# Optimization experiments

Hardware: AMD Instinct MI355X
Metric: run time of the kernel (lower is better)

Reference implementation:

```python
import jax, jax.numpy as jnp
import numpy as np

N_NODES = 50000
NUM_LAYERS = 3
D = 128
NUM_LABELS = 16
NUM_EDGES = 1600000


def setup_inputs() -> dict:
    key = jax.random.key(0)
    ks = jax.random.split(key, 6)
    s = 1.0 / np.sqrt(D)
    x = jax.random.normal(ks[0], (N_NODES, D), dtype=jnp.float32)
    edge_index = jax.random.randint(ks[1], (2, NUM_EDGES), 0, N_NODES, dtype=jnp.int64)
    W1 = jax.random.normal(ks[2], (NUM_LAYERS, D, D), dtype=jnp.float32) * s
    b1 = jnp.zeros((NUM_LAYERS, D), dtype=jnp.float32)
    W2 = jax.random.normal(ks[3], (NUM_LAYERS, D, D), dtype=jnp.float32) * s
    b2 = jnp.zeros((NUM_LAYERS, D), dtype=jnp.float32)
    Wc = jax.random.normal(ks[4], (D, NUM_LABELS), dtype=jnp.float32) * s
    bc = jnp.zeros((NUM_LABELS,), dtype=jnp.float32)
    return {"x": x, "edge_index": edge_index, "W1": W1, "b1": b1,
            "W2": W2, "b2": b2, "Wc": Wc, "bc": bc}


def reference(x, edge_index, W1, b1, W2, b2, Wc, bc):
    # PyG GINConv (default eps=0): h_i = MLP((1+eps)*x_i + sum_{j->i} x_j)
    src, dst = edge_index[0], edge_index[1]
    h = x
    for l in range(NUM_LAYERS):
        agg = jax.ops.segment_sum(h[src], dst, num_segments=N_NODES)  # [N, D]
        z = h + agg
        h = jax.nn.relu(z @ W1[l] + b1[l]) @ W2[l] + b2[l]
    logits = h @ Wc + bc
    return (h, logits)
```

## Files before the change

### kernel.cpp

```cpp
#include <hip/hip_runtime.h>

#define DD 128
#define CHUNK 6144
#define NBMAX 512
#define SCAP 8192

typedef __attribute__((ext_vector_type(8))) short bf16x8;
typedef __attribute__((ext_vector_type(4))) float f32x4;

__device__ __forceinline__ unsigned bf16rne(float f) {
  unsigned u = __float_as_uint(f);
  return (u + 0x7FFFu + ((u >> 16) & 1u)) >> 16;
}
__device__ __forceinline__ unsigned packbf(float lo, float hi) {
  return bf16rne(lo) | (bf16rne(hi) << 16);
}
__device__ __forceinline__ float bflo(unsigned v) { return __uint_as_float(v << 16); }
__device__ __forceinline__ float bfhi(unsigned v) { return __uint_as_float(v & 0xFFFF0000u); }

__device__ void block_scan_incl(int* cnt, int* inc, int nb, int tid) {
  for (int i = tid; i < nb; i += 256) inc[i] = cnt[i];
  __syncthreads();
  for (int d = 1; d < nb; d <<= 1) {
    int i0 = tid, i1 = tid + 256;
    int v0 = 0, v1 = 0;
    if (i0 < nb && i0 >= d) v0 = inc[i0 - d];
    if (i1 < nb && i1 >= d) v1 = inc[i1 - d];
    __syncthreads();
    if (i0 < nb) inc[i0] += v0;
    if (i1 < nb) inc[i1] += v1;
    __syncthreads();
  }
}

__global__ __launch_bounds__(256) void s1_hist(const int* __restrict__ dst,
                                               int* __restrict__ bucketCount, int e) {
  __shared__ int h[NBMAX];
  int tid = threadIdx.x;
  for (int i = tid; i < NBMAX; i += 256) h[i] = 0;
  __syncthreads();
  int i0 = blockIdx.x * CHUNK;
  int i1 = min(i0 + CHUNK, e);
  for (int i = i0 + tid; i < i1; i += 256) atomicAdd(&h[dst[i] >> 7], 1);
  __syncthreads();
  for (int i = tid; i < NBMAX; i += 256)
    if (h[i]) atomicAdd(&bucketCount[i], h[i]);
}

__global__ __launch_bounds__(256) void s2_scan(const int* __restrict__ bucketCount,
                                               int* __restrict__ bucketOff,
                                               int* __restrict__ gCursor,
                                               int* __restrict__ rs, int nb, int n, int e) {
  __shared__ int cnt[NBMAX], inc[NBMAX];
  int tid = threadIdx.x;
  for (int i = tid; i < nb; i += 256) cnt[i] = bucketCount[i];
  __syncthreads();
  block_scan_incl(cnt, inc, nb, tid);
  for (int i = tid; i < nb; i += 256) {
    int off = inc[i] - cnt[i];
    bucketOff[i] = off;
    gCursor[i] = off;
  }
  if (tid == 0) { bucketOff[nb] = e; rs[n] = e; }
}

__global__ __launch_bounds__(256) void s3_scatter(const int* __restrict__ src,
                                                  const int* __restrict__ dst,
                                                  int* __restrict__ gCursor,
                                                  unsigned int* __restrict__ bucketed,
                                                  int e, int nb) {
  __shared__ int cnt[NBMAX], inc[NBMAX], base[NBMAX], cur[NBMAX];
  __shared__ unsigned int pairs[CHUNK];
  int tid = threadIdx.x;
  for (int i = tid; i < nb; i += 256) cnt[i] = 0;
  __syncthreads();
  int i0 = blockIdx.x * CHUNK;
  int i1 = min(i0 + CHUNK, e);
  for (int i = i0 + tid; i < i1; i += 256) atomicAdd(&cnt[dst[i] >> 7], 1);
  __syncthreads();
  block_scan_incl(cnt, inc, nb, tid);
  for (int b = tid; b < nb; b += 256) {
    int c = cnt[b];
    base[b] = c ? atomicAdd(&gCursor[b], c) : 0;
    cur[b] = inc[b] - c;
  }
  __syncthreads();
  for (int i = i0 + tid; i < i1; i += 256) {
    int d = dst[i];
    int p = atomicAdd(&cur[d >> 7], 1);
    pairs[p] = (unsigned)d | ((unsigned)src[i] << 16);
  }
  __syncthreads();
  int m = i1 - i0;
  for (int i = tid; i < m; i += 256) {
    unsigned w = pairs[i];
    int b = (int)(w & 0xFFFFu) >> 7;
    bucketed[base[b] + (i - (inc[b] - cnt[b]))] = w;
  }
}

__global__ __launch_bounds__(256) void s4_fill(const unsigned int* __restrict__ bucketed,
                                               const int* __restrict__ bucketOff,
                                               int* __restrict__ rs,
                                               unsigned short* __restrict__ ssrc, int n) {
  __shared__ int cnt[128], inc[128], cur[128];
  __shared__ unsigned short outb[SCAP];
  int b = blockIdx.x;
  int bo = bucketOff[b], b1 = bucketOff[b + 1];
  int len = b1 - bo;
  int tid = threadIdx.x;
  int n0 = b << 7;
  if (tid < 128) cnt[tid] = 0;
  __syncthreads();
  for (int i = tid; i < len; i += 256) atomicAdd(&cnt[bucketed[bo + i] & 127], 1);
  __syncthreads();
  if (tid < 128) inc[tid] = cnt[tid];
  __syncthreads();
  for (int d = 1; d < 128; d <<= 1) {
    int v = 0;
    if (tid < 128 && tid >= d) v = inc[tid - d];
    __syncthreads();
    if (tid < 128) inc[tid] += v;
    __syncthreads();
  }
  if (tid < 128) {
    int off = inc[tid] - cnt[tid];
    cur[tid] = off;
    int node = n0 + tid;
    if (node < n) rs[node] = bo + off;
  }
  __syncthreads();
  if (len <= SCAP) {
    for (int i = tid; i < len; i += 256) {
      unsigned w = bucketed[bo + i];
      int p = atomicAdd(&cur[w & 127], 1);
      outb[p] = (unsigned short)(w >> 16);
    }
    __syncthreads();
    for (int i = tid; i < len; i += 256) ssrc[bo + i] = outb[i];
  } else {
    for (int i = tid; i < len; i += 256) {
      unsigned w = bucketed[bo + i];
      int p = atomicAdd(&cur[w & 127], 1);
      ssrc[bo + p] = (unsigned short)(w >> 16);
    }
  }
}

__global__ __launch_bounds__(256) void conv_bf16(const float* __restrict__ x,
                                                 unsigned int* __restrict__ hb, int n64) {
  int i = blockIdx.x * 256 + threadIdx.x;
  if (i < n64) {
    float2 v = ((const float2*)x)[i];
    hb[i] = packbf(v.x, v.y);
  }
}

__global__ __launch_bounds__(256) void prep_w(const float* __restrict__ W1,
                                              const float* __restrict__ W2,
                                              short* __restrict__ wt) {
  int idx = blockIdx.x * 256 + threadIdx.x;
  if (idx >= 3 * 2 * 16384) return;
  int lm = idx >> 14;
  int e = idx & 16383;
  int k = e >> 7;
  int col = e & 127;
  int layer = lm >> 1, mat = lm & 1;
  const float* W = mat ? W2 : W1;
  float w = W[layer * 16384 + k * 128 + col];
  unsigned short h = (unsigned short)bf16rne(w);
  float hv = __uint_as_float((unsigned)h << 16);
  unsigned short lo = (unsigned short)bf16rne(w - hv);
  size_t base = (size_t)lm * 2 * 16384;
  int ksw = k ^ ((col & 7) << 3);
  wt[base + col * 128 + ksw] = (short)h;
  wt[base + 16384 + col * 128 + ksw] = (short)lo;
}

__global__ __launch_bounds__(256) void gather_zb(const unsigned int* __restrict__ hb,
                                                 const int* __restrict__ rs,
                                                 const unsigned short* __restrict__ ssrc,
                                                 unsigned int* __restrict__ zb, int n) {
  int node = blockIdx.x * 4 + (threadIdx.x >> 6);
  if (node >= n) return;
  int lane = threadIdx.x & 63;
  int s0 = rs[node], s1 = rs[node + 1];
  unsigned v = hb[(size_t)node * 64 + lane];
  float ax = bflo(v), ay = bfhi(v);
  int last = s1 - 1;
  unsigned A[8], B[8];
#pragma unroll
  for (int i = 0; i < 8; ++i) {
    int t = s0 + i;
    unsigned val = hb[(size_t)ssrc[min(t, last)] * 64 + lane];
    A[i] = (t <= last) ? val : 0u;
  }
  for (int t = s0 + 8; t < s1; t += 8) {
#pragma unroll
    for (int i = 0; i < 8; ++i) {
      int u = t + i;
      unsigned val = hb[(size_t)ssrc[min(u, last)] * 64 + lane];
      B[i] = (u <= last) ? val : 0u;
    }
#pragma unroll
    for (int i = 0; i < 8; ++i) {
      ax += bflo(A[i]);
      ay += bfhi(A[i]);
    }
#pragma unroll
    for (int i = 0; i < 8; ++i) A[i] = B[i];
  }
#pragma unroll
  for (int i = 0; i < 8; ++i) {
    ax += bflo(A[i]);
    ay += bfhi(A[i]);
  }
  zb[(size_t)node * 64 + lane] = packbf(ax, ay);
}

__global__ __launch_bounds__(256, 2) void mlp_mfma(
    const unsigned int* __restrict__ zb,
    const short* __restrict__ Wt1, const short* __restrict__ Wt2,
    const float* __restrict__ b1, const float* __restrict__ b2,
    float* __restrict__ fout, unsigned short* __restrict__ hbout, int n) {
  __shared__ char wbuf[32768];
  __shared__ char hsb[128 * 256];
  int tid = threadIdx.x;
  int w = tid >> 6, lane = tid & 63;
  int lr = lane & 15, hi = lane >> 4;
  int wr = (w & 1) * 64;
  int wc = (w >> 1) * 64;
  int node0 = blockIdx.x * 128;

  bf16x8 a[4][4];
#pragma unroll
  for (int t = 0; t < 4; ++t) {
    int row = node0 + wr + t * 16 + lr;
    row = min(row, n - 1);
    const char* rp = (const char*)(zb + (size_t)row * 64);
#pragma unroll
    for (int ks = 0; ks < 4; ++ks)
      a[t][ks] = *(const bf16x8*)(rp + ks * 64 + hi * 16);
  }

  f32x4 acc[4][4];
#pragma unroll
  for (int ct = 0; ct < 4; ++ct) {
    float bb = b1[wc + ct * 16 + lr];
#pragma unroll
    for (int t = 0; t < 4; ++t) acc[t][ct] = (f32x4){bb, bb, bb, bb};
  }

#pragma unroll
  for (int p = 0; p < 2; ++p) {
    __syncthreads();
    {
      const char* gs = (const char*)(Wt1 + p * 16384);
      for (int i = tid * 16; i < 32768; i += 256 * 16)
        *(float4*)&wbuf[i] = *(const float4*)(gs + i);
    }
    __syncthreads();
#pragma unroll
    for (int ct = 0; ct < 4; ++ct) {
      int col = wc + ct * 16 + lr;
      int cx = (col & 7) << 4;
#pragma unroll
      for (int ks = 0; ks < 4; ++ks) {
        bf16x8 b = *(const bf16x8*)&wbuf[(col * 256 + ks * 64 + hi * 16) ^ cx];
#pragma unroll
        for (int t = 0; t < 4; ++t)
          acc[t][ct] = __builtin_amdgcn_mfma_f32_16x16x32_bf16(a[t][ks], b, acc[t][ct], 0, 0, 0);
      }
    }
  }

#pragma unroll
  for (int t = 0; t < 4; ++t)
#pragma unroll
    for (int ct = 0; ct < 4; ++ct)
#pragma unroll
      for (int r = 0; r < 4; ++r) {
        int row = wr + t * 16 + hi * 4 + r;
        int col = wc + ct * 16 + lr;
        float v = fmaxf(acc[t][ct][r], 0.f);
        int byte = (row * 256 + col * 2) ^ ((row & 7) << 4);
        *(unsigned short*)&hsb[byte] = (unsigned short)bf16rne(v);
      }
  __syncthreads();

  bf16x8 a2[4][4];
#pragma unroll
  for (int t = 0; t < 4; ++t) {
    int row = wr + t * 16 + lr;
    int xr = (row & 7) << 4;
#pragma unroll
    for (int ks = 0; ks < 4; ++ks)
      a2[t][ks] = *(const bf16x8*)&hsb[(row * 256 + ks * 64 + hi * 16) ^ xr];
  }

#pragma unroll
  for (int ct = 0; ct < 4; ++ct) {
    float bb = b2[wc + ct * 16 + lr];
#pragma unroll
    for (int t = 0; t < 4; ++t) acc[t][ct] = (f32x4){bb, bb, bb, bb};
  }

#pragma unroll
  for (int p = 0; p < 2; ++p) {
    __syncthreads();
    {
      const char* gs = (const char*)(Wt2 + p * 16384);
      for (int i = tid * 16; i < 32768; i += 256 * 16)
        *(float4*)&wbuf[i] = *(const float4*)(gs + i);
    }
    __syncthreads();
#pragma unroll
    for (int ct = 0; ct < 4; ++ct) {
      int col = wc + ct * 16 + lr;
      int cx = (col & 7) << 4;
#pragma unroll
      for (int ks = 0; ks < 4; ++ks) {
        bf16x8 b = *(const bf16x8*)&wbuf[(col * 256 + ks * 64 + hi * 16) ^ cx];
#pragma unroll
        for (int t = 0; t < 4; ++t)
          acc[t][ct] = __builtin_amdgcn_mfma_f32_16x16x32_bf16(a2[t][ks], b, acc[t][ct], 0, 0, 0);
      }
    }
  }

#pragma unroll
  for (int t = 0; t < 4; ++t)
#pragma unroll
    for (int ct = 0; ct < 4; ++ct)
#pragma unroll
      for (int r = 0; r < 4; ++r) {
        int node = node0 + wr + t * 16 + hi * 4 + r;
        if (node < n) {
          int col = wc + ct * 16 + lr;
          float v = acc[t][ct][r];
          if (fout) fout[(size_t)node * DD + col] = v;
          if (hbout) hbout[(size_t)node * DD + col] = (unsigned short)bf16rne(v);
        }
      }
}

__global__ __launch_bounds__(256) void classifier_k(const float* __restrict__ h,
                                                    const float* __restrict__ Wc,
                                                    const float* __restrict__ bc,
                                                    float* __restrict__ out, int n) {
  __shared__ float wcs[DD * 16];
  for (int i = threadIdx.x; i < DD * 16; i += 256) wcs[i] = Wc[i];
  __syncthreads();
  int t = blockIdx.x * 256 + threadIdx.x;
  int node = t >> 4, c = t & 15;
  if (node >= n) return;
  float acc = bc[c];
  const float* hr = h + (size_t)node * DD;
#pragma unroll 8
  for (int k = 0; k < DD; ++k) acc += hr[k] * wcs[k * 16 + c];
  out[(size_t)node * 16 + c] = acc;
}

extern "C" void kernel_launch(void* const* d_in, const int* in_sizes, int n_in,
                              void* d_out, int out_size, void* d_ws, size_t ws_size,
                              hipStream_t stream) {
  const float* x = (const float*)d_in[0];
  const int* ei = (const int*)d_in[1];
  const float* W1 = (const float*)d_in[2];
  const float* b1 = (const float*)d_in[3];
  const float* W2 = (const float*)d_in[4];
  const float* b2 = (const float*)d_in[5];
  const float* Wc = (const float*)d_in[6];
  const float* bc = (const float*)d_in[7];

  const int N = in_sizes[0] / DD;
  const int E = in_sizes[1] / 2;
  const int* src = ei;
  const int* dst = ei + E;
  const int NB = (N + 127) >> 7;

  float* outp = (float*)d_out;
  float* h_final = outp;
  float* logits = outp + (size_t)N * DD;

  char* ws = (char*)d_ws;
  size_t off = 0;
  auto alloc = [&](size_t bytes) {
    char* p = ws + off;
    off = (off + bytes + 255) & ~(size_t)255;
    return p;
  };
  unsigned int* zb = (unsigned int*)alloc((size_t)N * 64 * 4);
  unsigned int* hb = (unsigned int*)alloc((size_t)N * 64 * 4);
  short* wt = (short*)alloc((size_t)3 * 2 * 2 * 16384 * 2);
  int* bucketCount = (int*)alloc(NBMAX * 4);
  int* bucketOff = (int*)alloc((NBMAX + 1) * 4);
  int* gCursor = (int*)alloc(NBMAX * 4);
  int* rs = (int*)alloc((size_t)(N + 1) * 4);
  unsigned int* bucketed = (unsigned int*)alloc((size_t)E * 4);
  unsigned short* ssrc = (unsigned short*)alloc((size_t)E * 2);

  const int gEdge = (E + CHUNK - 1) / CHUNK;
  const int gGather = (N + 3) / 4;
  const int gMlp = (N + 127) / 128;

  hipMemsetAsync(bucketCount, 0, NBMAX * 4, stream);
  s1_hist<<<gEdge, 256, 0, stream>>>(dst, bucketCount, E);
  s2_scan<<<1, 256, 0, stream>>>(bucketCount, bucketOff, gCursor, rs, NB, N, E);
  s3_scatter<<<gEdge, 256, 0, stream>>>(src, dst, gCursor, bucketed, E, NB);
  s4_fill<<<NB, 256, 0, stream>>>(bucketed, bucketOff, rs, ssrc, N);

  prep_w<<<(3 * 2 * 16384 + 255) / 256, 256, 0, stream>>>(W1, W2, wt);
  conv_bf16<<<(N * 64 + 255) / 256, 256, 0, stream>>>(x, hb, N * 64);

  auto WT = [&](int layer, int mat) { return wt + ((size_t)(layer * 2 + mat)) * 2 * 16384; };

  gather_zb<<<gGather, 256, 0, stream>>>(hb, rs, ssrc, zb, N);
  mlp_mfma<<<gMlp, 256, 0, stream>>>(zb, WT(0, 0), WT(0, 1), b1, b2,
                                     nullptr, (unsigned short*)hb, N);
  gather_zb<<<gGather, 256, 0, stream>>>(hb, rs, ssrc, zb, N);
  mlp_mfma<<<gMlp, 256, 0, stream>>>(zb, WT(1, 0), WT(1, 1), b1 + DD, b2 + DD,
                                     nullptr, (unsigned short*)hb, N);
  gather_zb<<<gGather, 256, 0, stream>>>(hb, rs, ssrc, zb, N);
  mlp_mfma<<<gMlp, 256, 0, stream>>>(zb, WT(2, 0), WT(2, 1), b1 + 2 * DD, b2 + 2 * DD,
                                     h_final, nullptr, N);

  classifier_k<<<(N * 16 + 255) / 256, 256, 0, stream>>>(h_final, Wc, bc, logits, N);
}
```

Baseline: 294.4 us.

## Pad CSR rows to multiples of eight with a zero sentinel node, batch nodes per wave

The CSR neighbor lists are padded per node to a multiple of 8 (minimum 8) with a sentinel index pointing at an extra all-zero row in the bf16 feature buffer. The gather kernel can then drop the min/select bounds handling. Each wave now processes 8 consecutive nodes in turn, with row starts and padded degrees fetched once and broadcast by shuffle. The cost is extra sentinel loads for low-degree nodes, a larger ssrc buffer with per-bucket slack, and fewer waves in the gather launch.

```diff
diff --git a/kernel.cpp b/kernel.cpp
--- a/kernel.cpp
+++ b/kernel.cpp
@@ -4,6 +4,7 @@
 #define CHUNK 6144
 #define NBMAX 512
 #define SCAP 8192
+#define PADSLACK 1024
 
 typedef __attribute__((ext_vector_type(8))) short bf16x8;
 typedef __attribute__((ext_vector_type(4))) float f32x4;
@@ -102,57 +103,74 @@
 __global__ __launch_bounds__(256) void s4_fill(const unsigned int* __restrict__ bucketed,
                                                const int* __restrict__ bucketOff,
                                                int* __restrict__ rs,
+                                               unsigned short* __restrict__ pdeg,
                                                unsigned short* __restrict__ ssrc, int n) {
-  __shared__ int cnt[128], inc[128], cur[128];
+  __shared__ int cnt[128], pin[128], cur[128];
   __shared__ unsigned short outb[SCAP];
   int b = blockIdx.x;
   int bo = bucketOff[b], b1 = bucketOff[b + 1];
   int len = b1 - bo;
+  int pstart = bo + b * PADSLACK;
   int tid = threadIdx.x;
   int n0 = b << 7;
   if (tid < 128) cnt[tid] = 0;
   __syncthreads();
   for (int i = tid; i < len; i += 256) atomicAdd(&cnt[bucketed[bo + i] & 127], 1);
   __syncthreads();
-  if (tid < 128) inc[tid] = cnt[tid];
+  int pc = 0;
+  if (tid < 128) {
+    pc = max(8, (cnt[tid] + 7) & ~7);
+    pin[tid] = pc;
+  }
   __syncthreads();
   for (int d = 1; d < 128; d <<= 1) {
     int v = 0;
-    if (tid < 128 && tid >= d) v = inc[tid - d];
-    __syncthreads();
-    if (tid < 128) inc[tid] += v;
-    __syncthreads();
-  }
+    if (tid < 128 && tid >= d) v = pin[tid - d];
+    __syncthreads();
+    if (tid < 128) pin[tid] += v;
+    __syncthreads();
+  }
+  int plen = pin[127];
   if (tid < 128) {
-    int off = inc[tid] - cnt[tid];
+    int off = pin[tid] - pc;
     cur[tid] = off;
     int node = n0 + tid;
-    if (node < n) rs[node] = bo + off;
-  }
-  __syncthreads();
-  if (len <= SCAP) {
+    if (node < n) {
+      rs[node] = pstart + off;
+      pdeg[node] = (unsigned short)pc;
+    }
+  }
+  __syncthreads();
+  if (plen <= SCAP) {
+    for (int i = tid; i < plen; i += 256) outb[i] = (unsigned short)n;
+    __syncthreads();
     for (int i = tid; i < len; i += 256) {
       unsigned w = bucketed[bo + i];
       int p = atomicAdd(&cur[w & 127], 1);
       outb[p] = (unsigned short)(w >> 16);
     }
     __syncthreads();
-    for (int i = tid; i < len; i += 256) ssrc[bo + i] = outb[i];
+    for (int i = tid; i < plen; i += 256) ssrc[pstart + i] = outb[i];
   } else {
+    for (int i = tid; i < plen; i += 256) ssrc[pstart + i] = (unsigned short)n;
+    __syncthreads();
     for (int i = tid; i < len; i += 256) {
       unsigned w = bucketed[bo + i];
       int p = atomicAdd(&cur[w & 127], 1);
-      ssrc[bo + p] = (unsigned short)(w >> 16);
+      ssrc[pstart + p] = (unsigned short)(w >> 16);
     }
   }
 }
 
 __global__ __launch_bounds__(256) void conv_bf16(const float* __restrict__ x,
-                                                 unsigned int* __restrict__ hb, int n64) {
+                                                 unsigned int* __restrict__ hb,
+                                                 int n64, int total64) {
   int i = blockIdx.x * 256 + threadIdx.x;
   if (i < n64) {
     float2 v = ((const float2*)x)[i];
     hb[i] = packbf(v.x, v.y);
+  } else if (i < total64) {
+    hb[i] = 0u;
   }
 }
 
@@ -179,43 +197,51 @@
 
 __global__ __launch_bounds__(256) void gather_zb(const unsigned int* __restrict__ hb,
                                                  const int* __restrict__ rs,
+                                                 const unsigned short* __restrict__ pdeg,
                                                  const unsigned short* __restrict__ ssrc,
                                                  unsigned int* __restrict__ zb, int n) {
-  int node = blockIdx.x * 4 + (threadIdx.x >> 6);
-  if (node >= n) return;
+  int wv = blockIdx.x * 4 + (threadIdx.x >> 6);
+  int nodeBase = wv * 8;
+  if (nodeBase >= n) return;
   int lane = threadIdx.x & 63;
-  int s0 = rs[node], s1 = rs[node + 1];
-  unsigned v = hb[(size_t)node * 64 + lane];
-  float ax = bflo(v), ay = bfhi(v);
-  int last = s1 - 1;
-  unsigned A[8], B[8];
-#pragma unroll
-  for (int i = 0; i < 8; ++i) {
-    int t = s0 + i;
-    unsigned val = hb[(size_t)ssrc[min(t, last)] * 64 + lane];
-    A[i] = (t <= last) ? val : 0u;
-  }
-  for (int t = s0 + 8; t < s1; t += 8) {
-#pragma unroll
-    for (int i = 0; i < 8; ++i) {
-      int u = t + i;
-      unsigned val = hb[(size_t)ssrc[min(u, last)] * 64 + lane];
-      B[i] = (u <= last) ? val : 0u;
+  int myNode = nodeBase + (lane & 7);
+  int myRs = 0, myPd = 0;
+  if (myNode < n) {
+    myRs = rs[myNode];
+    myPd = pdeg[myNode];
+  }
+#pragma unroll 1
+  for (int u = 0; u < 8; ++u) {
+    int node = nodeBase + u;
+    if (node >= n) break;
+    int s0 = __shfl(myRs, u, 64);
+    int m = __shfl(myPd, u, 64);
+    unsigned v = hb[(unsigned)node * 64u + lane];
+    float ax = bflo(v), ay = bfhi(v);
+    unsigned A[8], B[8];
+#pragma unroll
+    for (int i = 0; i < 8; ++i)
+      A[i] = hb[(unsigned)ssrc[s0 + i] * 64u + lane];
+    int t1 = s0 + m;
+    for (int t = s0 + 8; t < t1; t += 8) {
+#pragma unroll
+      for (int i = 0; i < 8; ++i)
+        B[i] = hb[(unsigned)ssrc[t + i] * 64u + lane];
+#pragma unroll
+      for (int i = 0; i < 8; ++i) {
+        ax += bflo(A[i]);
+        ay += bfhi(A[i]);
+      }
+#pragma unroll
+      for (int i = 0; i < 8; ++i) A[i] = B[i];
     }
 #pragma unroll
     for (int i = 0; i < 8; ++i) {
       ax += bflo(A[i]);
       ay += bfhi(A[i]);
     }
-#pragma unroll
-    for (int i = 0; i < 8; ++i) A[i] = B[i];
-  }
-#pragma unroll
-  for (int i = 0; i < 8; ++i) {
-    ax += bflo(A[i]);
-    ay += bfhi(A[i]);
-  }
-  zb[(size_t)node * 64 + lane] = packbf(ax, ay);
+    zb[(unsigned)node * 64u + lane] = packbf(ax, ay);
+  }
 }
 
 __global__ __launch_bounds__(256, 2) void mlp_mfma(
@@ -391,37 +417,39 @@
     return p;
   };
   unsigned int* zb = (unsigned int*)alloc((size_t)N * 64 * 4);
-  unsigned int* hb = (unsigned int*)alloc((size_t)N * 64 * 4);
+  unsigned int* hb = (unsigned int*)alloc((size_t)(N + 1) * 64 * 4);
   short* wt = (short*)alloc((size_t)3 * 2 * 2 * 16384 * 2);
   int* bucketCount = (int*)alloc(NBMAX * 4);
   int* bucketOff = (int*)alloc((NBMAX + 1) * 4);
   int* gCursor = (int*)alloc(NBMAX * 4);
   int* rs = (int*)alloc((size_t)(N + 1) * 4);
+  unsigned short* pdeg = (unsigned short*)alloc((size_t)N * 2);
   unsigned int* bucketed = (unsigned int*)alloc((size_t)E * 4);
-  unsigned short* ssrc = (unsigned short*)alloc((size_t)E * 2);
+  unsigned short* ssrc = (unsigned short*)alloc(((size_t)E + (size_t)NB * PADSLACK) * 2);
 
   const int gEdge = (E + CHUNK - 1) / CHUNK;
-  const int gGather = (N + 3) / 4;
+  const int gGather = (N + 31) / 32;
   const int gMlp = (N + 127) / 128;
+  const int total64 = (N + 1) * 64;
 
   hipMemsetAsync(bucketCount, 0, NBMAX * 4, stream);
   s1_hist<<<gEdge, 256, 0, stream>>>(dst, bucketCount, E);
   s2_scan<<<1, 256, 0, stream>>>(bucketCount, bucketOff, gCursor, rs, NB, N, E);
   s3_scatter<<<gEdge, 256, 0, stream>>>(src, dst, gCursor, bucketed, E, NB);
-  s4_fill<<<NB, 256, 0, stream>>>(bucketed, bucketOff, rs, ssrc, N);
+  s4_fill<<<NB, 256, 0, stream>>>(bucketed, bucketOff, rs, pdeg, ssrc, N);
 
   prep_w<<<(3 * 2 * 16384 + 255) / 256, 256, 0, stream>>>(W1, W2, wt);
-  conv_bf16<<<(N * 64 + 255) / 256, 256, 0, stream>>>(x, hb, N * 64);
+  conv_bf16<<<(total64 + 255) / 256, 256, 0, stream>>>(x, hb, N * 64, total64);
 
   auto WT = [&](int layer, int mat) { return wt + ((size_t)(layer * 2 + mat)) * 2 * 16384; };
 
-  gather_zb<<<gGather, 256, 0, stream>>>(hb, rs, ssrc, zb, N);
+  gather_zb<<<gGather, 256, 0, stream>>>(hb, rs, pdeg, ssrc, zb, N);
   mlp_mfma<<<gMlp, 256, 0, stream>>>(zb, WT(0, 0), WT(0, 1), b1, b2,
                                      nullptr, (unsigned short*)hb, N);
-  gather_zb<<<gGather, 256, 0, stream>>>(hb, rs, ssrc, zb, N);
+  gather_zb<<<gGather, 256, 0, stream>>>(hb, rs, pdeg, ssrc, zb, N);
   mlp_mfma<<<gMlp, 256, 0, stream>>>(zb, WT(1, 0), WT(1, 1), b1 + DD, b2 + DD,
                                      nullptr, (unsigned short*)hb, N);
-  gather_zb<<<gGather, 256, 0, stream>>>(hb, rs, ssrc, zb, N);
+  gather_zb<<<gGather, 256, 0, stream>>>(hb, rs, pdeg, ssrc, zb, N);
   mlp_mfma<<<gMlp, 256, 0, stream>>>(zb, WT(2, 0), WT(2, 1), b1 + 2 * DD, b2 + 2 * DD,
                                      h_final, nullptr, N);
 
```

After: 321.2 us. 9.1% more time.
